# Performance work log

Hardware: AMD Instinct MI355X
Metric: run time of the kernel (lower is better)

## Reference

```python
import jax, jax.numpy as jnp
import numpy as np

WORD_VOCAB = 100000
TAG_VOCAB = 60
DW = 300   # word embed dim
DT = 50    # tag embed dim
H = 300    # hidden size
DEPTH = 13
N_NODES = 2 ** DEPTH - 1      # 8191
N_LEAVES = 2 ** (DEPTH - 1)   # 4096


def setup_inputs() -> dict:
    key = jax.random.key(0)
    ks = jax.random.split(key, 10)
    scale = 0.05
    return {
        "leaf_word_ids": jax.random.randint(ks[0], (N_LEAVES,), 0, WORD_VOCAB, dtype=jnp.int32),
        # tag ids laid out level-by-level, leaves first, root last
        "tag_ids": jax.random.randint(ks[1], (N_NODES,), 0, TAG_VOCAB, dtype=jnp.int32),
        "word_table": jax.random.normal(ks[2], (WORD_VOCAB, DW), jnp.float32) * scale,
        "tag_table": jax.random.normal(ks[3], (TAG_VOCAB, DT), jnp.float32) * scale,
        "Wr": jax.random.normal(ks[4], (DW + DT + 2 * H, H), jnp.float32) * scale,
        "br": jnp.zeros((H,), jnp.float32),
        "Wz": jax.random.normal(ks[5], (DW + DT + 2 * H, H), jnp.float32) * scale,
        "bz": jnp.zeros((H,), jnp.float32),
        "Wu": jax.random.normal(ks[6], (DW + 2 * H, H), jnp.float32) * scale,
        "bu": jnp.zeros((H,), jnp.float32),
    }


def reference(leaf_word_ids, tag_ids, word_table, tag_table, Wr, br, Wz, bz, Wu, bu):
    """Labeled binary tree GRU over a complete binary tree, batched by depth.

    Leaves (which carry words) are processed first with zero child states,
    then each internal level combines adjacent child pairs, exactly the
    per-node math of LabeledBinaryTreeGRU.node_forward.
    """
    h_dim = Wr.shape[1]
    dw = word_table.shape[1]
    dtype = word_table.dtype

    def gru(we, te, lh, rh):
        # we:[m,DW] te:[m,DT] lh,rh:[m,H]
        x = jnp.concatenate([we, te, lh, rh], axis=1)
        r = jax.nn.sigmoid(x @ Wr + br)
        z = jax.nn.sigmoid(x @ Wz + bz)
        u = jnp.tanh(jnp.concatenate([we, r * lh, r * rh], axis=1) @ Wu + bu)
        return z * (lh + rh) + (1.0 - z) * u

    n_leaf = leaf_word_ids.shape[0]
    # leaf level: real word embeddings, zero child states
    we = word_table[leaf_word_ids]
    te = tag_table[tag_ids[:n_leaf]]
    zeros_h = jnp.zeros((n_leaf, h_dim), dtype)
    h = gru(we, te, zeros_h, zeros_h)
    outputs = [h]

    off = n_leaf
    m = n_leaf // 2
    while m >= 1:
        lh = h[0::2]   # left children of this level's parents
        rh = h[1::2]   # right children
        te = tag_table[tag_ids[off:off + m]]
        we = jnp.zeros((m, dw), dtype)  # internal nodes have no word (node.idx is None)
        h = gru(we, te, lh, rh)
        outputs.append(h)
        off += m
        m //= 2

    outputs = jnp.concatenate(outputs, axis=0)  # [N_NODES, H]
    final_state = h                              # [1, H] root state
    return outputs, final_state
```

## Files before the change

kernel.cpp:

```cpp
#include <hip/hip_runtime.h>
#include <math.h>

#define H 300
#define NLEAF 4096

typedef unsigned int  uint;
typedef unsigned short ushort;
typedef __attribute__((ext_vector_type(8))) short  short8;
typedef __attribute__((ext_vector_type(4))) float  f32x4;

__device__ __forceinline__ float sigmoidf_(float x) { return 1.0f / (1.0f + expf(-x)); }

__device__ __forceinline__ ushort f2bf(float f)
{
    uint u = __float_as_uint(f);
    u += 0x7FFF + ((u >> 16) & 1);
    return (ushort)(u >> 16);
}
__device__ __forceinline__ uint2 pack4(float4 v)
{
    uint2 w;
    w.x = (uint)f2bf(v.x) | ((uint)f2bf(v.y) << 16);
    w.y = (uint)f2bf(v.z) | ((uint)f2bf(v.w) << 16);
    return w;
}

template<int NT, int KSTEPS, int KT, int AS>
__device__ __forceinline__ void mfma_gemm(const ushort* A_lds, const ushort* __restrict__ Bt,
                                          int tile0, int s0, int lane, f32x4* acc)
{
    const ushort* Ap = A_lds + (lane & 15) * AS + ((lane >> 4) * 8) + s0 * 32;
    const ushort* Bp[NT];
    #pragma unroll
    for (int t = 0; t < NT; ++t)
        Bp[t] = Bt + ((long)(tile0 + t) * KT + s0) * 512 + lane * 8;

    short8 aA, aB, bA[NT], bB[NT];
    aA = *(const short8*)Ap;
    #pragma unroll
    for (int t = 0; t < NT; ++t) bA[t] = *(const short8*)Bp[t];

    int s = 0;
    #pragma unroll 1
    for (; s + 2 < KSTEPS; s += 2) {
        aB = *(const short8*)(Ap + (s + 1) * 32);
        #pragma unroll
        for (int t = 0; t < NT; ++t) bB[t] = *(const short8*)(Bp[t] + (s + 1) * 512);
        #pragma unroll
        for (int t = 0; t < NT; ++t)
            acc[t] = __builtin_amdgcn_mfma_f32_16x16x32_bf16(aA, bA[t], acc[t], 0, 0, 0);
        aA = *(const short8*)(Ap + (s + 2) * 32);
        #pragma unroll
        for (int t = 0; t < NT; ++t) bA[t] = *(const short8*)(Bp[t] + (s + 2) * 512);
        #pragma unroll
        for (int t = 0; t < NT; ++t)
            acc[t] = __builtin_amdgcn_mfma_f32_16x16x32_bf16(aB, bB[t], acc[t], 0, 0, 0);
    }
    if (KSTEPS - s == 2) {
        aB = *(const short8*)(Ap + (s + 1) * 32);
        #pragma unroll
        for (int t = 0; t < NT; ++t) bB[t] = *(const short8*)(Bp[t] + (s + 1) * 512);
        #pragma unroll
        for (int t = 0; t < NT; ++t)
            acc[t] = __builtin_amdgcn_mfma_f32_16x16x32_bf16(aA, bA[t], acc[t], 0, 0, 0);
        #pragma unroll
        for (int t = 0; t < NT; ++t)
            acc[t] = __builtin_amdgcn_mfma_f32_16x16x32_bf16(aB, bB[t], acc[t], 0, 0, 0);
    } else {
        #pragma unroll
        for (int t = 0; t < NT; ++t)
            acc[t] = __builtin_amdgcn_mfma_f32_16x16x32_bf16(aA, bA[t], acc[t], 0, 0, 0);
    }
}

__global__ __launch_bounds__(256) void prep_k(
    const float* __restrict__ Wr, const float* __restrict__ Wz,
    const float* __restrict__ Wu, const float* __restrict__ tag_table,
    const float* __restrict__ br, const float* __restrict__ bz,
    ushort* __restrict__ WArzT, ushort* __restrict__ WuTpT, ushort* __restrict__ WLzuT,
    float* __restrict__ tag_r, float* __restrict__ tag_z)
{
    __shared__ float te[50];
    int b = blockIdx.x;
    int tid = threadIdx.x;
    if (b < 640) {
        int c = b;
        int tile = c >> 4, cl = c & 15;
        int gate = (c >= 320);
        int cc = gate ? c - 320 : c;
        const float* WA = gate ? Wz : Wr;
        for (int o = tid; o < 76; o += 256) {
            int k0 = o * 8;
            ushort tmp[8];
            #pragma unroll
            for (int i = 0; i < 8; ++i) {
                int k = k0 + i;
                float v = 0.f;
                if (cc < 300) {
                    if (k < 300) v = WA[(350 + k) * H + cc];
                    else if (k >= 304 && k < 604) v = WA[(k + 346) * H + cc];
                }
                tmp[i] = f2bf(v);
            }
            int s = k0 >> 5, kk0 = k0 & 31;
            long pos = ((long)(tile * 19 + s)) * 512 + ((kk0 >> 3) * 16 + cl) * 8;
            uint4 w;
            w.x = (uint)tmp[0] | ((uint)tmp[1] << 16);
            w.y = (uint)tmp[2] | ((uint)tmp[3] << 16);
            w.z = (uint)tmp[4] | ((uint)tmp[5] << 16);
            w.w = (uint)tmp[6] | ((uint)tmp[7] << 16);
            *(uint4*)&WArzT[pos] = w;
        }
        const float* WL = gate ? Wu : Wz;
        for (int o = tid; o < 40; o += 256) {
            int k0 = o * 8;
            ushort tmp[8];
            #pragma unroll
            for (int i = 0; i < 8; ++i) {
                int k = k0 + i;
                float v = (cc < 300 && k < 300) ? WL[k * H + cc] : 0.f;
                tmp[i] = f2bf(v);
            }
            int s = k0 >> 5, kk0 = k0 & 31;
            long pos = ((long)(tile * 10 + s)) * 512 + ((kk0 >> 3) * 16 + cl) * 8;
            uint4 w;
            w.x = (uint)tmp[0] | ((uint)tmp[1] << 16);
            w.y = (uint)tmp[2] | ((uint)tmp[3] << 16);
            w.z = (uint)tmp[4] | ((uint)tmp[5] << 16);
            w.w = (uint)tmp[6] | ((uint)tmp[7] << 16);
            *(uint4*)&WLzuT[pos] = w;
        }
        if (c < 320) {
            for (int o = tid; o < 76; o += 256) {
                int k0 = o * 8;
                ushort tmp[8];
                #pragma unroll
                for (int i = 0; i < 8; ++i) {
                    int k = k0 + i;
                    float v = 0.f;
                    if (c < 300) {
                        if (k < 300) v = Wu[(300 + k) * H + c];
                        else if (k >= 304 && k < 604) v = Wu[(k + 296) * H + c];
                    }
                    tmp[i] = f2bf(v);
                }
                int s = k0 >> 5, kk0 = k0 & 31;
                long pos = ((long)(tile * 19 + s)) * 512 + ((kk0 >> 3) * 16 + cl) * 8;
                uint4 w;
                w.x = (uint)tmp[0] | ((uint)tmp[1] << 16);
                w.y = (uint)tmp[2] | ((uint)tmp[3] << 16);
                w.z = (uint)tmp[4] | ((uint)tmp[5] << 16);
                w.w = (uint)tmp[6] | ((uint)tmp[7] << 16);
                *(uint4*)&WuTpT[pos] = w;
            }
        }
    } else {
        int t = b - 640;
        if (tid < 50) te[tid] = tag_table[t * 50 + tid];
        __syncthreads();
        for (int k = tid; k < H; k += 256) {
            float ar = br[k], az = bz[k];
            #pragma unroll 10
            for (int j = 0; j < 50; ++j) {
                float tv = te[j];
                ar = fmaf(tv, Wr[(H + j) * H + k], ar);
                az = fmaf(tv, Wz[(H + j) * H + k], az);
            }
            tag_r[t * H + k] = ar;
            tag_z[t * H + k] = az;
        }
    }
}

__global__ __launch_bounds__(512, 1) void leaf_mfma_k(
    const int* __restrict__ word_ids, const int* __restrict__ tag_ids,
    const float* __restrict__ word_table, const ushort* __restrict__ WLzuT,
    const float* __restrict__ bu, const float* __restrict__ tag_z,
    float* __restrict__ out)
{
    __shared__ ushort Abf[16 * 328];
    __shared__ float zbuf[16][304];
    int tid = threadIdx.x;
    int node0 = blockIdx.x * 16;

    for (int idx = tid; idx < 16 * 82; idx += 512) {
        int j = idx / 82, q = idx - j * 82;
        char* rowb = (char*)(Abf + j * 328);
        if (q < 75) {
            float4 v = ((const float4*)(word_table + (long)word_ids[node0 + j] * H))[q];
            *(uint2*)(rowb + q * 8) = pack4(v);
        } else {
            *(uint2*)(rowb + q * 8) = make_uint2(0u, 0u);
        }
    }
    __syncthreads();

    int wv = tid >> 6, lane = tid & 63;
    int jrow = (lane >> 4) * 4;

    f32x4 acc[5];
    #pragma unroll
    for (int t = 0; t < 5; ++t) acc[t] = (f32x4)(0.f);

    if (wv < 4) {
        mfma_gemm<5, 10, 10, 328>(Abf, WLzuT, wv * 5, 0, lane, acc);
        int tg[4];
        #pragma unroll
        for (int q = 0; q < 4; ++q) tg[q] = tag_ids[node0 + jrow + q];
        #pragma unroll
        for (int t = 0; t < 5; ++t) {
            int c = wv * 80 + t * 16 + (lane & 15);
            #pragma unroll
            for (int q = 0; q < 4; ++q)
                if (c < 300) zbuf[jrow + q][c] = sigmoidf_(acc[t][q] + tag_z[tg[q] * H + c]);
        }
    } else {
        mfma_gemm<5, 10, 10, 328>(Abf, WLzuT, 20 + (wv - 4) * 5, 0, lane, acc);
    }
    __syncthreads();
    if (wv >= 4) {
        #pragma unroll
        for (int t = 0; t < 5; ++t) {
            int c = (wv - 4) * 80 + t * 16 + (lane & 15);
            #pragma unroll
            for (int q = 0; q < 4; ++q) {
                if (c < 300) {
                    int jn = jrow + q;
                    float u = tanhf(acc[t][q] + bu[c]);
                    out[(long)(node0 + jn) * H + c] = (1.f - zbuf[jn][c]) * u;
                }
            }
        }
    }
}

__device__ __forceinline__ void fused_body(
    const int* __restrict__ tag_ids, const ushort* __restrict__ WArzT,
    const ushort* __restrict__ WuTpT, const float* __restrict__ bu,
    const float* __restrict__ tag_r, const float* __restrict__ tag_z,
    float* __restrict__ out, int off, int prevOff, int m,
    int node0, int tid, ushort* Abf, float (*zbuf)[304], float (*pbuf)[64][21])
{
    for (int idx = tid; idx < 16 * 154; idx += 512) {
        int j = idx / 154, q = idx - j * 154;
        char* rowb = (char*)(Abf + j * 616);
        bool valid = (node0 + j) < m;
        if (q < 75) {
            uint2 w = make_uint2(0u, 0u);
            if (valid) {
                float4 v = ((const float4*)(out + (long)(prevOff + 2 * (node0 + j)) * H))[q];
                w = pack4(v);
            }
            *(uint2*)(rowb + q * 8) = w;
        } else if (q < 150) {
            int qq = q - 75;
            uint2 w = make_uint2(0u, 0u);
            if (valid) {
                float4 v = ((const float4*)(out + (long)(prevOff + 2 * (node0 + j) + 1) * H))[qq];
                w = pack4(v);
            }
            *(uint2*)(rowb + 608 + qq * 8) = w;
        } else {
            int pb = (q == 150) ? 600 : (1208 + (q - 151) * 8);
            *(uint2*)(rowb + pb) = make_uint2(0u, 0u);
        }
    }
    __syncthreads();

    int wv = tid >> 6, lane = tid & 63;
    int jrow = (lane >> 4) * 4;
    int tg[4];
    #pragma unroll
    for (int q = 0; q < 4; ++q) {
        int gn = node0 + jrow + q;
        tg[q] = tag_ids[off + (gn < m ? gn : 0)];
    }

    f32x4 accG[5];
    #pragma unroll
    for (int t = 0; t < 5; ++t) accG[t] = (f32x4)(0.f);
    mfma_gemm<5, 19, 19, 616>(Abf, WArzT, wv * 5, 0, lane, accG);
    __syncthreads();

    float Sr[5][4];
    if (wv < 4) {
        #pragma unroll
        for (int t = 0; t < 5; ++t) {
            int c = wv * 80 + t * 16 + (lane & 15);
            #pragma unroll
            for (int q = 0; q < 4; ++q) {
                int jn = jrow + q, gn = node0 + jn;
                if (c < 300 && gn < m) {
                    float lh = out[(long)(prevOff + 2 * gn) * H + c];
                    float rh = out[(long)(prevOff + 2 * gn + 1) * H + c];
                    float r  = sigmoidf_(accG[t][q] + tag_r[tg[q] * H + c]);
                    Sr[t][q] = lh + rh;
                    Abf[jn * 616 + c]       = f2bf(r * lh);
                    Abf[jn * 616 + 304 + c] = f2bf(r * rh);
                }
            }
        }
    } else {
        #pragma unroll
        for (int t = 0; t < 5; ++t) {
            int cz = (wv - 4) * 80 + t * 16 + (lane & 15);
            #pragma unroll
            for (int q = 0; q < 4; ++q) {
                int jn = jrow + q, gn = node0 + jn;
                if (cz < 300 && gn < m)
                    zbuf[jn][cz] = sigmoidf_(accG[t][q] + tag_z[tg[q] * H + cz]);
            }
        }
    }
    __syncthreads();

    f32x4 accU[5];
    #pragma unroll
    for (int t = 0; t < 5; ++t) accU[t] = (f32x4)(0.f);
    if (wv < 4) {
        mfma_gemm<5, 10, 19, 616>(Abf, WuTpT, wv * 5, 0, lane, accU);
    } else {
        mfma_gemm<5, 9, 19, 616>(Abf, WuTpT, (wv - 4) * 5, 10, lane, accU);
        #pragma unroll
        for (int t = 0; t < 5; ++t)
            #pragma unroll
            for (int q = 0; q < 4; ++q)
                pbuf[wv - 4][lane][t * 4 + q] = accU[t][q];
    }
    __syncthreads();
    if (wv < 4) {
        #pragma unroll
        for (int t = 0; t < 5; ++t) {
            int c = wv * 80 + t * 16 + (lane & 15);
            #pragma unroll
            for (int q = 0; q < 4; ++q) {
                int jn = jrow + q, gn = node0 + jn;
                if (c < 300 && gn < m) {
                    float a = accU[t][q] + pbuf[wv][lane][t * 4 + q];
                    float u = tanhf(a + bu[c]);
                    float z = zbuf[jn][c];
                    out[(long)(off + gn) * H + c] = z * Sr[t][q] + (1.f - z) * u;
                }
            }
        }
    }
}

__global__ __launch_bounds__(512, 1) void level_fused_k(
    const int* __restrict__ tag_ids, const ushort* __restrict__ WArzT,
    const ushort* __restrict__ WuTpT, const float* __restrict__ bu,
    const float* __restrict__ tag_r, const float* __restrict__ tag_z,
    float* __restrict__ out, int off, int prevOff, int m)
{
    __shared__ ushort Abf[16 * 616];
    __shared__ float zbuf[16][304];
    __shared__ float pbuf[4][64][21];
    fused_body(tag_ids, WArzT, WuTpT, bu, tag_r, tag_z, out, off, prevOff, m,
               blockIdx.x * 16, threadIdx.x, Abf, zbuf, pbuf);
}

__global__ __launch_bounds__(256, 1) void split_gates_k(
    const int* __restrict__ tag_ids, const ushort* __restrict__ WArzT,
    const float* __restrict__ tag_r, const float* __restrict__ tag_z,
    const float* __restrict__ out,
    float* __restrict__ zws, float* __restrict__ Sws, ushort* __restrict__ rxws,
    int off, int prevOff, int m)
{
    __shared__ ushort Abf[16 * 616];
    __shared__ float pbuf[3][64][20];
    int tid = threadIdx.x;
    int mt = blockIdx.x >> 3, cb = blockIdx.x & 7;
    int node0 = mt * 16;

    for (int idx = tid; idx < 16 * 154; idx += 256) {
        int j = idx / 154, q = idx - j * 154;
        char* rowb = (char*)(Abf + j * 616);
        bool valid = (node0 + j) < m;
        if (q < 75) {
            uint2 w = make_uint2(0u, 0u);
            if (valid) {
                float4 v = ((const float4*)(out + (long)(prevOff + 2 * (node0 + j)) * H))[q];
                w = pack4(v);
            }
            *(uint2*)(rowb + q * 8) = w;
        } else if (q < 150) {
            int qq = q - 75;
            uint2 w = make_uint2(0u, 0u);
            if (valid) {
                float4 v = ((const float4*)(out + (long)(prevOff + 2 * (node0 + j) + 1) * H))[qq];
                w = pack4(v);
            }
            *(uint2*)(rowb + 608 + qq * 8) = w;
        } else {
            int pb = (q == 150) ? 600 : (1208 + (q - 151) * 8);
            *(uint2*)(rowb + pb) = make_uint2(0u, 0u);
        }
    }
    __syncthreads();

    int wv = tid >> 6, lane = tid & 63;
    int tile0 = cb * 5;
    f32x4 acc[5];
    #pragma unroll
    for (int t = 0; t < 5; ++t) acc[t] = (f32x4)(0.f);
    if (wv == 0)      mfma_gemm<5, 5, 19, 616>(Abf, WArzT, tile0, 0,  lane, acc);
    else if (wv == 1) mfma_gemm<5, 5, 19, 616>(Abf, WArzT, tile0, 5,  lane, acc);
    else if (wv == 2) mfma_gemm<5, 5, 19, 616>(Abf, WArzT, tile0, 10, lane, acc);
    else              mfma_gemm<5, 4, 19, 616>(Abf, WArzT, tile0, 15, lane, acc);
    if (wv > 0) {
        #pragma unroll
        for (int t = 0; t < 5; ++t)
            #pragma unroll
            for (int q = 0; q < 4; ++q)
                pbuf[wv - 1][lane][t * 4 + q] = acc[t][q];
    }
    __syncthreads();
    if (wv == 0) {
        int jrow = (lane >> 4) * 4;
        #pragma unroll
        for (int t = 0; t < 5; ++t) {
            int c = cb * 80 + t * 16 + (lane & 15);
            #pragma unroll
            for (int q = 0; q < 4; ++q) {
                int jn = jrow + q, gn = node0 + jn;
                float a = acc[t][q] + pbuf[0][lane][t * 4 + q]
                        + pbuf[1][lane][t * 4 + q] + pbuf[2][lane][t * 4 + q];
                if (c < 320) {
                    if (c < 300 && gn < m) {
                        int tg = tag_ids[off + gn];
                        float r  = sigmoidf_(a + tag_r[tg * H + c]);
                        float lh = out[(long)(prevOff + 2 * gn) * H + c];
                        float rh = out[(long)(prevOff + 2 * gn + 1) * H + c];
                        Sws[gn * 304 + c] = lh + rh;
                        rxws[(long)gn * 608 + c]       = f2bf(r * lh);
                        rxws[(long)gn * 608 + 304 + c] = f2bf(r * rh);
                    } else if (c >= 300 && c < 304 && gn < m) {
                        rxws[(long)gn * 608 + c]       = 0;
                        rxws[(long)gn * 608 + 304 + c] = 0;
                    }
                } else {
                    int cz = c - 320;
                    if (cz < 300 && gn < m) {
                        int tg = tag_ids[off + gn];
                        zws[gn * 304 + cz] = sigmoidf_(a + tag_z[tg * H + cz]);
                    }
                }
            }
        }
    }
}

__global__ __launch_bounds__(256, 1) void split_u_k(
    const ushort* __restrict__ WuTpT, const float* __restrict__ bu,
    const float* __restrict__ zws, const float* __restrict__ Sws,
    const ushort* __restrict__ rxws,
    float* __restrict__ out, int off, int m, float* __restrict__ dup)
{
    __shared__ ushort Abf[16 * 616];
    __shared__ float pbuf[3][64][20];
    int tid = threadIdx.x;
    int mt = blockIdx.x >> 2, ub = blockIdx.x & 3;
    int node0 = mt * 16;

    for (int idx = tid; idx < 16 * 77; idx += 256) {
        int j = idx / 77, q = idx - j * 77;
        uint4* dst = (uint4*)(Abf + j * 616) + q;
        if (q < 76 && (node0 + j) < m)
            *dst = ((const uint4*)(rxws + (long)(node0 + j) * 608))[q];
        else
            *dst = make_uint4(0u, 0u, 0u, 0u);
    }
    __syncthreads();

    int wv = tid >> 6, lane = tid & 63;
    int tile0 = ub * 5;
    f32x4 acc[5];
    #pragma unroll
    for (int t = 0; t < 5; ++t) acc[t] = (f32x4)(0.f);
    if (wv == 0)      mfma_gemm<5, 5, 19, 616>(Abf, WuTpT, tile0, 0,  lane, acc);
    else if (wv == 1) mfma_gemm<5, 5, 19, 616>(Abf, WuTpT, tile0, 5,  lane, acc);
    else if (wv == 2) mfma_gemm<5, 5, 19, 616>(Abf, WuTpT, tile0, 10, lane, acc);
    else              mfma_gemm<5, 4, 19, 616>(Abf, WuTpT, tile0, 15, lane, acc);
    if (wv > 0) {
        #pragma unroll
        for (int t = 0; t < 5; ++t)
            #pragma unroll
            for (int q = 0; q < 4; ++q)
                pbuf[wv - 1][lane][t * 4 + q] = acc[t][q];
    }
    __syncthreads();
    if (wv == 0) {
        int jrow = (lane >> 4) * 4;
        #pragma unroll
        for (int t = 0; t < 5; ++t) {
            int c = ub * 80 + t * 16 + (lane & 15);
            #pragma unroll
            for (int q = 0; q < 4; ++q) {
                int jn = jrow + q, gn = node0 + jn;
                if (c < 300 && gn < m) {
                    float a = acc[t][q] + pbuf[0][lane][t * 4 + q]
                            + pbuf[1][lane][t * 4 + q] + pbuf[2][lane][t * 4 + q];
                    float u = tanhf(a + bu[c]);
                    float z = zws[gn * 304 + c];
                    float h = z * Sws[gn * 304 + c] + (1.f - z) * u;
                    out[(long)(off + gn) * H + c] = h;
                    if (dup && gn == 0) dup[c] = h;
                }
            }
        }
    }
}

extern "C" void kernel_launch(void* const* d_in, const int* in_sizes, int n_in,
                              void* d_out, int out_size, void* d_ws, size_t ws_size,
                              hipStream_t stream)
{
    const int*   word_ids   = (const int*)  d_in[0];
    const int*   tag_ids    = (const int*)  d_in[1];
    const float* word_table = (const float*)d_in[2];
    const float* tag_table  = (const float*)d_in[3];
    const float* Wr         = (const float*)d_in[4];
    const float* br         = (const float*)d_in[5];
    const float* Wz         = (const float*)d_in[6];
    const float* bz         = (const float*)d_in[7];
    const float* Wu         = (const float*)d_in[8];
    const float* bu         = (const float*)d_in[9];
    float* out = (float*)d_out;

    float* tag_r = (float*)d_ws;
    float* tag_z = tag_r + 18000;
    float* zws   = tag_z + 18000;
    float* Sws   = zws + 128 * 304;
    ushort* rxws = (ushort*)(Sws + 128 * 304);
    ushort* WArzT = rxws + 128L * 608;
    ushort* WuTpT = WArzT + 40L * 19 * 512;
    ushort* WLzuT = WuTpT + 20L * 19 * 512;

    prep_k<<<700, 256, 0, stream>>>(Wr, Wz, Wu, tag_table, br, bz,
                                    WArzT, WuTpT, WLzuT, tag_r, tag_z);

    leaf_mfma_k<<<NLEAF / 16, 512, 0, stream>>>(
        word_ids, tag_ids, word_table, WLzuT, bu, tag_z, out);

    float* finalDup = out + (long)8191 * H;
    int off = NLEAF, prevOff = 0;
    for (int m = 2048; m >= 1; m >>= 1) {
        if (m >= 256) {
            level_fused_k<<<m / 16, 512, 0, stream>>>(
                tag_ids, WArzT, WuTpT, bu, tag_r, tag_z, out, off, prevOff, m);
        } else {
            int nMt = (m + 15) / 16;
            split_gates_k<<<nMt * 8, 256, 0, stream>>>(
                tag_ids, WArzT, tag_r, tag_z, out, zws, Sws, rxws, off, prevOff, m);
            split_u_k<<<nMt * 4, 256, 0, stream>>>(
                WuTpT, bu, zws, Sws, rxws, out, off, m, (m == 1) ? finalDup : nullptr);
        }
        prevOff = off;
        off += m;
    }
}
```

Baseline: 313.9 us.

## Merge small-level gate/update kernels into one persistent chain kernel with flag sync

Replaces the 16 separate launches for the tree levels with m<=128 with a single kernel of 228 blocks. Each block takes a role (gates or update) for a given level and spins on per-stage atomic counters in global memory before running that stage. Flags are zeroed in prep_k. The aim is to remove kernel launch and drain gaps on the latency-bound tail of the tree. The cost is spin-wait overhead, and it relies on all 228 blocks being co-resident so the waits cannot deadlock.

```diff
diff --git a/kernel.cpp b/kernel.cpp
--- a/kernel.cpp
+++ b/kernel.cpp
@@ -78,7 +78,7 @@
     const float* __restrict__ Wu, const float* __restrict__ tag_table,
     const float* __restrict__ br, const float* __restrict__ bz,
     ushort* __restrict__ WArzT, ushort* __restrict__ WuTpT, ushort* __restrict__ WLzuT,
-    float* __restrict__ tag_r, float* __restrict__ tag_z)
+    float* __restrict__ tag_r, float* __restrict__ tag_z, uint* __restrict__ flags)
 {
     __shared__ float te[50];
     int b = blockIdx.x;
@@ -156,6 +156,9 @@
         }
     } else {
         int t = b - 640;
+        if (b == 640) {
+            for (int i = tid; i < 512; i += 256) flags[i] = 0u;
+        }
         if (tid < 50) te[tid] = tag_table[t * 50 + tid];
         __syncthreads();
         for (int k = tid; k < H; k += 256) {
@@ -359,19 +362,15 @@
                blockIdx.x * 16, threadIdx.x, Abf, zbuf, pbuf);
 }
 
-__global__ __launch_bounds__(256, 1) void split_gates_k(
+__device__ __forceinline__ void gates_body(
     const int* __restrict__ tag_ids, const ushort* __restrict__ WArzT,
     const float* __restrict__ tag_r, const float* __restrict__ tag_z,
     const float* __restrict__ out,
     float* __restrict__ zws, float* __restrict__ Sws, ushort* __restrict__ rxws,
-    int off, int prevOff, int m)
-{
-    __shared__ ushort Abf[16 * 616];
-    __shared__ float pbuf[3][64][20];
-    int tid = threadIdx.x;
-    int mt = blockIdx.x >> 3, cb = blockIdx.x & 7;
+    int off, int prevOff, int m, int mt, int cb, int tid,
+    ushort* Abf, float (*pbuf)[64][20])
+{
     int node0 = mt * 16;
-
     for (int idx = tid; idx < 16 * 154; idx += 256) {
         int j = idx / 154, q = idx - j * 154;
         char* rowb = (char*)(Abf + j * 616);
@@ -450,18 +449,14 @@
     }
 }
 
-__global__ __launch_bounds__(256, 1) void split_u_k(
+__device__ __forceinline__ void u_body(
     const ushort* __restrict__ WuTpT, const float* __restrict__ bu,
     const float* __restrict__ zws, const float* __restrict__ Sws,
     const ushort* __restrict__ rxws,
-    float* __restrict__ out, int off, int m, float* __restrict__ dup)
-{
-    __shared__ ushort Abf[16 * 616];
-    __shared__ float pbuf[3][64][20];
-    int tid = threadIdx.x;
-    int mt = blockIdx.x >> 2, ub = blockIdx.x & 3;
+    float* __restrict__ out, int off, int m, float* __restrict__ dup,
+    int mt, int ub, int tid, ushort* Abf, float (*pbuf)[64][20])
+{
     int node0 = mt * 16;
-
     for (int idx = tid; idx < 16 * 77; idx += 256) {
         int j = idx / 77, q = idx - j * 77;
         uint4* dst = (uint4*)(Abf + j * 616) + q;
@@ -511,6 +506,57 @@
     }
 }
 
+__global__ __launch_bounds__(256, 1) void chain_k(
+    const int* __restrict__ tag_ids, const ushort* __restrict__ WArzT,
+    const ushort* __restrict__ WuTpT, const float* __restrict__ bu,
+    const float* __restrict__ tag_r, const float* __restrict__ tag_z,
+    float* __restrict__ out,
+    float* __restrict__ zws, float* __restrict__ Sws, ushort* __restrict__ rxws,
+    uint* __restrict__ flags, float* __restrict__ finalDup)
+{
+    __shared__ ushort Abf[16 * 616];
+    __shared__ float pbuf[3][64][20];
+    const int GBt[8] = {64, 32, 16, 8, 8, 8, 8, 8};
+    const int UBt[8] = {32, 16, 8, 4, 4, 4, 4, 4};
+    const int offT[8] = {7936, 8064, 8128, 8160, 8176, 8184, 8188, 8190};
+
+    int b = (int)blockIdx.x;
+    int li = 0, role = 0, local = 0;
+    for (int i = 0; i < 8; ++i) {
+        if (b < GBt[i]) { li = i; role = 0; local = b; break; }
+        b -= GBt[i];
+        if (b < UBt[i]) { li = i; role = 1; local = b; break; }
+        b -= UBt[i];
+    }
+    int m = 128 >> li;
+    int off = offT[li], prevOff = off - 2 * m;
+
+    if (!(role == 0 && li == 0)) {
+        int wIdx = (role == 0) ? (2 * li - 1) : (2 * li);
+        uint wCnt = (role == 0) ? (uint)UBt[li - 1] : (uint)GBt[li];
+        if (threadIdx.x == 0) {
+            while (__hip_atomic_load(&flags[wIdx * 32], __ATOMIC_RELAXED,
+                                     __HIP_MEMORY_SCOPE_AGENT) < wCnt)
+                __builtin_amdgcn_s_sleep(8);
+        }
+        __syncthreads();
+        __threadfence();
+    }
+
+    if (role == 0)
+        gates_body(tag_ids, WArzT, tag_r, tag_z, out, zws, Sws, rxws,
+                   off, prevOff, m, local >> 3, local & 7, threadIdx.x, Abf, pbuf);
+    else
+        u_body(WuTpT, bu, zws, Sws, rxws, out, off, m,
+               (li == 7) ? finalDup : nullptr, local >> 2, local & 3,
+               threadIdx.x, Abf, pbuf);
+
+    __syncthreads();
+    __threadfence();
+    if (threadIdx.x == 0)
+        atomicAdd(&flags[(2 * li + role) * 32], 1u);
+}
+
 extern "C" void kernel_launch(void* const* d_in, const int* in_sizes, int n_in,
                               void* d_out, int out_size, void* d_ws, size_t ws_size,
                               hipStream_t stream)
@@ -535,27 +581,23 @@
     ushort* WArzT = rxws + 128L * 608;
     ushort* WuTpT = WArzT + 40L * 19 * 512;
     ushort* WLzuT = WuTpT + 20L * 19 * 512;
+    uint*  flags  = (uint*)(WLzuT + 40L * 10 * 512);
 
     prep_k<<<700, 256, 0, stream>>>(Wr, Wz, Wu, tag_table, br, bz,
-                                    WArzT, WuTpT, WLzuT, tag_r, tag_z);
+                                    WArzT, WuTpT, WLzuT, tag_r, tag_z, flags);
 
     leaf_mfma_k<<<NLEAF / 16, 512, 0, stream>>>(
         word_ids, tag_ids, word_table, WLzuT, bu, tag_z, out);
 
-    float* finalDup = out + (long)8191 * H;
     int off = NLEAF, prevOff = 0;
-    for (int m = 2048; m >= 1; m >>= 1) {
-        if (m >= 256) {
-            level_fused_k<<<m / 16, 512, 0, stream>>>(
-                tag_ids, WArzT, WuTpT, bu, tag_r, tag_z, out, off, prevOff, m);
-        } else {
-            int nMt = (m + 15) / 16;
-            split_gates_k<<<nMt * 8, 256, 0, stream>>>(
-                tag_ids, WArzT, tag_r, tag_z, out, zws, Sws, rxws, off, prevOff, m);
-            split_u_k<<<nMt * 4, 256, 0, stream>>>(
-                WuTpT, bu, zws, Sws, rxws, out, off, m, (m == 1) ? finalDup : nullptr);
-        }
+    for (int m = 2048; m >= 256; m >>= 1) {
+        level_fused_k<<<m / 16, 512, 0, stream>>>(
+            tag_ids, WArzT, WuTpT, bu, tag_r, tag_z, out, off, prevOff, m);
         prevOff = off;
         off += m;
     }
-}
+
+    float* finalDup = out + (long)8191 * H;
+    chain_k<<<228, 256, 0, stream>>>(
+        tag_ids, WArzT, WuTpT, bu, tag_r, tag_z, out, zws, Sws, rxws, flags, finalDup);
+}
```

Result: slower. 350.1 us (+11.5%).
